# Kernel optimization log

Hardware: AMD Instinct MI355X
Metric: run time of the kernel (lower is better)

The kernel has to match this reference:

```python
import jax, jax.numpy as jnp
import numpy as np
import math

GROUP = 64
DIM = 4096


def _hadamard(group):
    # normalized Hadamard matrix via Sylvester construction, matching constructH
    H = np.ones((1, 1), dtype=np.float32)
    for _ in range(int(math.log2(group))):
        H = np.block([[H, H], [H, -H]]) / math.sqrt(2)
    return jnp.asarray(H)


def setup_inputs() -> dict:
    key = jax.random.key(0)
    x = jax.random.normal(key, (4, 4096, DIM), dtype=jnp.float32)
    # learnable parameter: Hadamard block repeated dim//group times -> [dim/group, group, group]
    H = jnp.broadcast_to(_hadamard(GROUP), (DIM // GROUP, GROUP, GROUP)).copy()
    return {"x": x, "H": H}


def reference(x, H):
    # x: [..., dim] -> view tokens as [N, dim/group, group], apply per-block matmul by H
    x_shape = x.shape
    n_blocks, group = H.shape[0], H.shape[1]
    xb = x.reshape(-1, n_blocks, group)            # [N, G, g]
    yb = jnp.einsum('ngk,gkh->ngh', xb, H)          # block-diagonal transform
    return yb.reshape(x_shape)
```

## Files before the change

kernel.cpp:

```cpp
#include <hip/hip_runtime.h>
#include <hip/hip_bf16.h>


#define DIM 4096
#define NG   64
#define GSZ  64
#define TOK_PER_BLK 256

typedef __bf16 bf16x8 __attribute__((ext_vector_type(8)));
typedef float  f32x4  __attribute__((ext_vector_type(4)));

__global__ __launch_bounds__(256, 8)
void hh_mfma_kernel(const float* __restrict__ x, const float* __restrict__ H,
                    float* __restrict__ y, int ntok) {
    __shared__ __align__(16) float Hl[GSZ * GSZ];

    const int g    = blockIdx.x & (NG - 1);
    const int tb   = blockIdx.x >> 6;
    const int tid  = threadIdx.x;
    const int lane = tid & 63;
    const int wave = tid >> 6;

    const float* __restrict__ Hg = H + (size_t)g * (GSZ * GSZ);
    #pragma unroll
    for (int i = 0; i < 4; ++i) {
        int idx = tid + i * 256;
        ((f32x4*)Hl)[idx] = ((const f32x4*)Hg)[idx];
    }
    __syncthreads();

    const int hcol = lane & 15;
    const int hrow = (lane >> 4) * 8;
    bf16x8 hfrag[2][4];
    #pragma unroll
    for (int kt = 0; kt < 2; ++kt)
        #pragma unroll
        for (int ht = 0; ht < 4; ++ht)
            #pragma unroll
            for (int i = 0; i < 8; ++i)
                hfrag[kt][ht][i] =
                    (__bf16)Hl[(kt * 32 + hrow + i) * GSZ + ht * 16 + hcol];

    const int tokl  = lane & 15;
    const int acolk = (lane >> 4) * 8;
    const int hq    = (lane >> 4) * 4;

    const int tok0 = tb * TOK_PER_BLK + wave * 64;

    #pragma unroll
    for (int tt = 0; tt < 4; ++tt) {
        const int tbase = tok0 + tt * 16;

        bf16x8 xfrag[2];
        const float* __restrict__ xp =
            x + (size_t)(tbase + tokl) * DIM + g * GSZ + acolk;
        #pragma unroll
        for (int kt = 0; kt < 2; ++kt) {
            f32x4 lo = *(const f32x4*)(xp + kt * 32);
            f32x4 hi = *(const f32x4*)(xp + kt * 32 + 4);
            #pragma unroll
            for (int i = 0; i < 4; ++i) {
                xfrag[kt][i]     = (__bf16)lo[i];
                xfrag[kt][i + 4] = (__bf16)hi[i];
            }
        }

        f32x4 acc[4];
        #pragma unroll
        for (int ht = 0; ht < 4; ++ht) {
            acc[ht] = (f32x4){0.f, 0.f, 0.f, 0.f};
            acc[ht] = __builtin_amdgcn_mfma_f32_16x16x32_bf16(
                          hfrag[0][ht], xfrag[0], acc[ht], 0, 0, 0);
            acc[ht] = __builtin_amdgcn_mfma_f32_16x16x32_bf16(
                          hfrag[1][ht], xfrag[1], acc[ht], 0, 0, 0);
        }

        float* __restrict__ yp =
            y + (size_t)(tbase + tokl) * DIM + g * GSZ + hq;
        #pragma unroll
        for (int ht = 0; ht < 4; ++ht)
            __builtin_nontemporal_store(acc[ht], (f32x4*)(yp + ht * 16));
    }
}

extern "C" void kernel_launch(void* const* d_in, const int* in_sizes, int n_in,
                              void* d_out, int out_size, void* d_ws, size_t ws_size,
                              hipStream_t stream) {
    const float* x = (const float*)d_in[0];
    const float* H = (const float*)d_in[1];
    float* y = (float*)d_out;

    const int ntok = in_sizes[0] / DIM;
    const int nblk = (ntok / TOK_PER_BLK) * NG;

    hipLaunchKernelGGL(hh_mfma_kernel, dim3(nblk), dim3(256), 0, stream,
                       x, H, y, ntok);
}
```

Measured before the change: 99.84 us.

## Double-buffer x loads, drop LDS staging of H, double tokens per block

Each wave now handles 8 token tiles instead of 4, and the x loads for the next tile are issued before the current tile's MFMAs run, a software double-buffer in registers. H fragments are read straight from global memory instead of being staged through shared memory, which removes the LDS copy and the barrier. Launch bounds drop to 4 blocks per CU, allowing more registers. The risks are lower occupancy, fewer blocks overall, and uncoalesced global gathers of H.

Measured after the change: 98.93 us. About the same (-0.9%).

```diff
diff --git a/kernel.cpp b/kernel.cpp
--- a/kernel.cpp
+++ b/kernel.cpp
@@ -5,32 +5,23 @@
 #define DIM 4096
 #define NG   64
 #define GSZ  64
-#define TOK_PER_BLK 256
+#define TOK_PER_BLK 512
+#define TILES 8
 
 typedef __bf16 bf16x8 __attribute__((ext_vector_type(8)));
 typedef float  f32x4  __attribute__((ext_vector_type(4)));
 
-__global__ __launch_bounds__(256, 8)
+__global__ __launch_bounds__(256, 4)
 void hh_mfma_kernel(const float* __restrict__ x, const float* __restrict__ H,
                     float* __restrict__ y, int ntok) {
-    __shared__ __align__(16) float Hl[GSZ * GSZ];
-
     const int g    = blockIdx.x & (NG - 1);
     const int tb   = blockIdx.x >> 6;
-    const int tid  = threadIdx.x;
-    const int lane = tid & 63;
-    const int wave = tid >> 6;
-
-    const float* __restrict__ Hg = H + (size_t)g * (GSZ * GSZ);
-    #pragma unroll
-    for (int i = 0; i < 4; ++i) {
-        int idx = tid + i * 256;
-        ((f32x4*)Hl)[idx] = ((const f32x4*)Hg)[idx];
-    }
-    __syncthreads();
+    const int lane = threadIdx.x & 63;
+    const int wave = threadIdx.x >> 6;
 
     const int hcol = lane & 15;
     const int hrow = (lane >> 4) * 8;
+    const float* __restrict__ Hg = H + (size_t)g * (GSZ * GSZ);
     bf16x8 hfrag[2][4];
     #pragma unroll
     for (int kt = 0; kt < 2; ++kt)
@@ -39,31 +30,45 @@
             #pragma unroll
             for (int i = 0; i < 8; ++i)
                 hfrag[kt][ht][i] =
-                    (__bf16)Hl[(kt * 32 + hrow + i) * GSZ + ht * 16 + hcol];
+                    (__bf16)Hg[(kt * 32 + hrow + i) * GSZ + ht * 16 + hcol];
 
     const int tokl  = lane & 15;
     const int acolk = (lane >> 4) * 8;
     const int hq    = (lane >> 4) * 4;
 
-    const int tok0 = tb * TOK_PER_BLK + wave * 64;
+    const int tok0 = tb * TOK_PER_BLK + wave * (16 * TILES);
+    const float* __restrict__ xb =
+        x + (size_t)(tok0 + tokl) * DIM + g * GSZ + acolk;
+    float* __restrict__ yb =
+        y + (size_t)(tok0 + tokl) * DIM + g * GSZ + hq;
+
+    f32x4 raw[2][4];
 
     #pragma unroll
-    for (int tt = 0; tt < 4; ++tt) {
-        const int tbase = tok0 + tt * 16;
+    for (int kt = 0; kt < 2; ++kt) {
+        raw[0][kt * 2 + 0] = *(const f32x4*)(xb + kt * 32);
+        raw[0][kt * 2 + 1] = *(const f32x4*)(xb + kt * 32 + 4);
+    }
+
+    #pragma unroll
+    for (int tt = 0; tt < TILES; ++tt) {
+        if (tt + 1 < TILES) {
+            const float* __restrict__ xp = xb + (size_t)(tt + 1) * 16 * DIM;
+            #pragma unroll
+            for (int kt = 0; kt < 2; ++kt) {
+                raw[(tt + 1) & 1][kt * 2 + 0] = *(const f32x4*)(xp + kt * 32);
+                raw[(tt + 1) & 1][kt * 2 + 1] = *(const f32x4*)(xp + kt * 32 + 4);
+            }
+        }
 
         bf16x8 xfrag[2];
-        const float* __restrict__ xp =
-            x + (size_t)(tbase + tokl) * DIM + g * GSZ + acolk;
         #pragma unroll
-        for (int kt = 0; kt < 2; ++kt) {
-            f32x4 lo = *(const f32x4*)(xp + kt * 32);
-            f32x4 hi = *(const f32x4*)(xp + kt * 32 + 4);
+        for (int kt = 0; kt < 2; ++kt)
             #pragma unroll
             for (int i = 0; i < 4; ++i) {
-                xfrag[kt][i]     = (__bf16)lo[i];
-                xfrag[kt][i + 4] = (__bf16)hi[i];
+                xfrag[kt][i]     = (__bf16)raw[tt & 1][kt * 2 + 0][i];
+                xfrag[kt][i + 4] = (__bf16)raw[tt & 1][kt * 2 + 1][i];
             }
-        }
 
         f32x4 acc[4];
         #pragma unroll
@@ -75,8 +80,7 @@
                           hfrag[1][ht], xfrag[1], acc[ht], 0, 0, 0);
         }
 
-        float* __restrict__ yp =
-            y + (size_t)(tbase + tokl) * DIM + g * GSZ + hq;
+        float* __restrict__ yp = yb + (size_t)tt * 16 * DIM;
         #pragma unroll
         for (int ht = 0; ht < 4; ++ht)
             __builtin_nontemporal_store(acc[ht], (f32x4*)(yp + ht * 16));
```
